# Kernel optimization log

Hardware: AMD Instinct MI355X
Metric: run time of the kernel (lower is better)

Reference implementation:

```python
import jax, jax.numpy as jnp
import numpy as np

HIDDEN = 16
N_CLASSES = 10
N_NODES = 100000
N_EDGES = 3200000
D_FEAT = 128
NEG_SLOPE = 0.1


def setup_inputs() -> dict:
    key = jax.random.key(0)
    k1, k2, k3 = jax.random.split(key, 3)
    features = jax.random.normal(k1, (N_NODES, D_FEAT), dtype=jnp.float32)
    edge_src = jax.random.randint(k2, (N_EDGES,), 0, N_NODES, dtype=jnp.int64)
    edge_dst = jax.random.randint(k3, (N_EDGES,), 0, N_NODES, dtype=jnp.int64)
    return {"features": features, "edge_src": edge_src, "edge_dst": edge_dst}


def reference(features, edge_src, edge_dst):
    # SpMM: h[v] = sum over edges (u->v) of features[u]   (binary adjacency)
    msgs = features[edge_src]                      # [E, F] irregular gather
    h = jax.ops.segment_sum(msgs, edge_dst, num_segments=N_NODES)  # [N, F]
    # x @ ones(F, HIDDEN): every column equals the row-sum of h
    r1 = jnp.sum(h, axis=-1)                       # [N]
    a1 = jax.nn.leaky_relu(r1, NEG_SLOPE)          # leaky relu, slope 0.1
    # x @ ones(HIDDEN, N_CLASSES): each class column = HIDDEN * a1
    r2 = HIDDEN * a1
    a2 = jax.nn.leaky_relu(r2, NEG_SLOPE)
    # x @ ones(N_CLASSES, 1) then .int() and flatten
    r3 = N_CLASSES * a2                            # [N]
    return r3.astype(jnp.int32).reshape(-1)
```

## Files before the change

kernel.cpp:

```cpp
#include <hip/hip_runtime.h>

#define N_NODES  100000
#define N_EDGES  3200000
#define D_FEAT   128
#define SLICE    33344
#define SLICE4   (SLICE / 4)
#define N_SLICES 3
#define MAX_B    85
#define EPT      8
#define TPB      1024
#define STRIDE   (TPB * EPT)

__device__ __forceinline__ unsigned short f2bf(float f) {
    union { float f; unsigned u; } c; c.f = f;
    unsigned r = c.u + 0x7FFFu + ((c.u >> 16) & 1u);
    return (unsigned short)(r >> 16);
}
__device__ __forceinline__ float bf2f(unsigned short h) {
    union { unsigned u; float f; } c; c.u = ((unsigned)h) << 16; return c.f;
}

__global__ void __launch_bounds__(256) rowsum_kernel(
    const float* __restrict__ feat,
    float* __restrict__ rowsum)
{
    const int gid = (int)(blockIdx.x * blockDim.x + threadIdx.x);
    const int row = gid >> 5;
    const int sub = gid & 31;
    if (row >= N_NODES) return;

    const float4 v = reinterpret_cast<const float4*>(
        feat + (size_t)row * D_FEAT)[sub];
    float s = (v.x + v.y) + (v.z + v.w);

    #pragma unroll
    for (int off = 16; off > 0; off >>= 1)
        s += __shfl_xor(s, off, 64);

    if (sub == 0) rowsum[row] = s;
}

__global__ void __launch_bounds__(TPB) scatter_kernel(
    const int* __restrict__ edge_src,
    const int* __restrict__ edge_dst,
    const float* __restrict__ rowsum,
    unsigned short* __restrict__ copies,
    int B, int epb)
{
    __shared__ float lds[SLICE];

    const int tid = (int)threadIdx.x;
    const int b   = (int)blockIdx.x;
    const int s   = (int)blockIdx.y;
    const int lo  = s * SLICE;
    const unsigned len = (unsigned)((N_NODES - lo < SLICE) ? (N_NODES - lo) : SLICE);

    float4 z; z.x = z.y = z.z = z.w = 0.0f;
    for (int i = tid; i < SLICE4; i += TPB)
        reinterpret_cast<float4*>(lds)[i] = z;
    __syncthreads();

    const int begin = b * epb;
    const int end   = (begin + epb < N_EDGES) ? begin + epb : N_EDGES;

    int eA = begin + tid * EPT;
    int eB = eA + STRIDE;

    int4 dA0, dA1, sA0, sA1, dB0, dB1, sB0, sB1;
    if (eA     < end) { dA0 = *(const int4*)(edge_dst + eA);     sA0 = *(const int4*)(edge_src + eA); }
    if (eA + 4 < end) { dA1 = *(const int4*)(edge_dst + eA + 4); sA1 = *(const int4*)(edge_src + eA + 4); }
    if (eB     < end) { dB0 = *(const int4*)(edge_dst + eB);     sB0 = *(const int4*)(edge_src + eB); }
    if (eB + 4 < end) { dB1 = *(const int4*)(edge_dst + eB + 4); sB1 = *(const int4*)(edge_src + eB + 4); }

    unsigned jA0, jA1, jA2, jA3, jA4, jA5, jA6, jA7;
    float    wA0, wA1, wA2, wA3, wA4, wA5, wA6, wA7;
    {
        const bool v0 = (eA < end), v1 = (eA + 4 < end);
        jA0 = v0 ? (unsigned)(dA0.x - lo) : 0xFFFFFFFFu;
        jA1 = v0 ? (unsigned)(dA0.y - lo) : 0xFFFFFFFFu;
        jA2 = v0 ? (unsigned)(dA0.z - lo) : 0xFFFFFFFFu;
        jA3 = v0 ? (unsigned)(dA0.w - lo) : 0xFFFFFFFFu;
        jA4 = v1 ? (unsigned)(dA1.x - lo) : 0xFFFFFFFFu;
        jA5 = v1 ? (unsigned)(dA1.y - lo) : 0xFFFFFFFFu;
        jA6 = v1 ? (unsigned)(dA1.z - lo) : 0xFFFFFFFFu;
        jA7 = v1 ? (unsigned)(dA1.w - lo) : 0xFFFFFFFFu;
        wA0 = (jA0 < len) ? rowsum[sA0.x] : 0.0f;
        wA1 = (jA1 < len) ? rowsum[sA0.y] : 0.0f;
        wA2 = (jA2 < len) ? rowsum[sA0.z] : 0.0f;
        wA3 = (jA3 < len) ? rowsum[sA0.w] : 0.0f;
        wA4 = (jA4 < len) ? rowsum[sA1.x] : 0.0f;
        wA5 = (jA5 < len) ? rowsum[sA1.y] : 0.0f;
        wA6 = (jA6 < len) ? rowsum[sA1.z] : 0.0f;
        wA7 = (jA7 < len) ? rowsum[sA1.w] : 0.0f;
    }

    while (eA < end) {
        const int eC = eB + STRIDE;
        int4 dC0, dC1, sC0, sC1;
        if (eC     < end) { dC0 = *(const int4*)(edge_dst + eC);     sC0 = *(const int4*)(edge_src + eC); }
        if (eC + 4 < end) { dC1 = *(const int4*)(edge_dst + eC + 4); sC1 = *(const int4*)(edge_src + eC + 4); }

        const bool v0 = (eB < end), v1 = (eB + 4 < end);
        unsigned jB0 = v0 ? (unsigned)(dB0.x - lo) : 0xFFFFFFFFu;
        unsigned jB1 = v0 ? (unsigned)(dB0.y - lo) : 0xFFFFFFFFu;
        unsigned jB2 = v0 ? (unsigned)(dB0.z - lo) : 0xFFFFFFFFu;
        unsigned jB3 = v0 ? (unsigned)(dB0.w - lo) : 0xFFFFFFFFu;
        unsigned jB4 = v1 ? (unsigned)(dB1.x - lo) : 0xFFFFFFFFu;
        unsigned jB5 = v1 ? (unsigned)(dB1.y - lo) : 0xFFFFFFFFu;
        unsigned jB6 = v1 ? (unsigned)(dB1.z - lo) : 0xFFFFFFFFu;
        unsigned jB7 = v1 ? (unsigned)(dB1.w - lo) : 0xFFFFFFFFu;
        float wB0 = (jB0 < len) ? rowsum[sB0.x] : 0.0f;
        float wB1 = (jB1 < len) ? rowsum[sB0.y] : 0.0f;
        float wB2 = (jB2 < len) ? rowsum[sB0.z] : 0.0f;
        float wB3 = (jB3 < len) ? rowsum[sB0.w] : 0.0f;
        float wB4 = (jB4 < len) ? rowsum[sB1.x] : 0.0f;
        float wB5 = (jB5 < len) ? rowsum[sB1.y] : 0.0f;
        float wB6 = (jB6 < len) ? rowsum[sB1.z] : 0.0f;
        float wB7 = (jB7 < len) ? rowsum[sB1.w] : 0.0f;

        if (jA0 < len) atomicAdd(&lds[jA0], wA0);
        if (jA1 < len) atomicAdd(&lds[jA1], wA1);
        if (jA2 < len) atomicAdd(&lds[jA2], wA2);
        if (jA3 < len) atomicAdd(&lds[jA3], wA3);
        if (jA4 < len) atomicAdd(&lds[jA4], wA4);
        if (jA5 < len) atomicAdd(&lds[jA5], wA5);
        if (jA6 < len) atomicAdd(&lds[jA6], wA6);
        if (jA7 < len) atomicAdd(&lds[jA7], wA7);

        eA = eB; eB = eC;
        dB0 = dC0; dB1 = dC1; sB0 = sC0; sB1 = sC1;
        jA0 = jB0; jA1 = jB1; jA2 = jB2; jA3 = jB3;
        jA4 = jB4; jA5 = jB5; jA6 = jB6; jA7 = jB7;
        wA0 = wB0; wA1 = wB1; wA2 = wB2; wA3 = wB3;
        wA4 = wB4; wA5 = wB5; wA6 = wB6; wA7 = wB7;
    }
    __syncthreads();

    unsigned short* __restrict__ dstp = copies + ((size_t)s * B + b) * SLICE;
    const int len4 = (int)len >> 2;
    for (int i = tid; i < len4; i += TPB) {
        const float4 v = reinterpret_cast<const float4*>(lds)[i];
        ushort4 o;
        o.x = f2bf(v.x); o.y = f2bf(v.y); o.z = f2bf(v.z); o.w = f2bf(v.w);
        reinterpret_cast<ushort4*>(dstp)[i] = o;
    }
}

__global__ void __launch_bounds__(256) reduce_final_kernel(
    const unsigned short* __restrict__ copies,
    int B,
    int* __restrict__ out)
{
    const int i4 = (int)(blockIdx.x * blockDim.x + threadIdx.x);
    if (i4 >= N_NODES / 4) return;

    const int s  = (i4 >= 2 * SLICE4) ? 2 : (i4 >= SLICE4 ? 1 : 0);
    const int j4 = i4 - s * SLICE4;

    float ax = 0.0f, ay = 0.0f, az = 0.0f, aw = 0.0f;
    const ushort4* base = reinterpret_cast<const ushort4*>(copies)
                        + (size_t)s * B * SLICE4 + j4;
    #pragma unroll 4
    for (int c = 0; c < B; ++c) {
        const ushort4 v = base[(size_t)c * SLICE4];
        ax += bf2f(v.x); ay += bf2f(v.y); az += bf2f(v.z); aw += bf2f(v.w);
    }

    auto act = [](float x) -> int {
        const float a1 = (x  > 0.0f) ? x  : 0.1f * x;
        const float r2 = 16.0f * a1;
        const float a2 = (r2 > 0.0f) ? r2 : 0.1f * r2;
        return (int)(10.0f * a2);
    };

    int4 o;
    o.x = act(ax); o.y = act(ay); o.z = act(az); o.w = act(aw);
    reinterpret_cast<int4*>(out)[i4] = o;
}

extern "C" void kernel_launch(void* const* d_in, const int* in_sizes, int n_in,
                              void* d_out, int out_size, void* d_ws, size_t ws_size,
                              hipStream_t stream)
{
    const float* feat     = (const float*)d_in[0];
    const int*   edge_src = (const int*)d_in[1];
    const int*   edge_dst = (const int*)d_in[2];
    int*         out      = (int*)d_out;

    float* rowsum = (float*)d_ws;
    unsigned short* copies = (unsigned short*)(rowsum + N_NODES);

    size_t avail = (ws_size > (size_t)N_NODES * 4) ? ws_size - (size_t)N_NODES * 4 : 0;
    int B = (int)(avail / ((size_t)N_SLICES * SLICE * 2));
    if (B > MAX_B) B = MAX_B;
    if (B < 1) B = 1;

    int epb = (N_EDGES + B - 1) / B;
    epb = (epb + 7) & ~7;

    {
        const int threads = 256;
        const long long total = (long long)N_NODES * 32;
        const int blocks = (int)((total + threads - 1) / threads);
        rowsum_kernel<<<blocks, threads, 0, stream>>>(feat, rowsum);
    }

    {
        dim3 grid(B, N_SLICES);
        scatter_kernel<<<grid, TPB, 0, stream>>>(edge_src, edge_dst, rowsum,
                                                 copies, B, epb);
    }

    {
        const int threads = 256;
        const int blocks = (N_NODES / 4 + threads - 1) / threads;
        reduce_final_kernel<<<blocks, threads, 0, stream>>>(copies, B, out);
    }
}
```

Measured before the change: 53.18 us.

## Fix chunk count at 80 and remap scatter blocks so XCDs share edge chunks

Replaces the workspace-derived chunk count with a fixed 80 chunks of 40000 edges, launched as a 1D grid of 240 blocks. Block IDs are remapped so the three slice blocks that read the same edge chunk land on the same XCD (round-robin dispatch of 8), meant to let them share that XCD's L2 for the edge and rowsum reads. Constant loop bounds in the reduce kernel also allow full compile-time trip counts. The change drops the ws_size check, so it assumes the workspace is large enough, and fewer chunks means more edges per block.

Result: faster. 50.93 us (-4.2%).

```diff
diff --git a/kernel.cpp b/kernel.cpp
--- a/kernel.cpp
+++ b/kernel.cpp
@@ -6,7 +6,8 @@
 #define SLICE    33344
 #define SLICE4   (SLICE / 4)
 #define N_SLICES 3
-#define MAX_B    85
+#define NCHUNK   80
+#define EPB      40000
 #define EPT      8
 #define TPB      1024
 #define STRIDE   (TPB * EPT)
@@ -44,15 +45,18 @@
     const int* __restrict__ edge_src,
     const int* __restrict__ edge_dst,
     const float* __restrict__ rowsum,
-    unsigned short* __restrict__ copies,
-    int B, int epb)
+    unsigned short* __restrict__ copies)
 {
     __shared__ float lds[SLICE];
 
-    const int tid = (int)threadIdx.x;
-    const int b   = (int)blockIdx.x;
-    const int s   = (int)blockIdx.y;
-    const int lo  = s * SLICE;
+    const int tid  = (int)threadIdx.x;
+    const int bid  = (int)blockIdx.x;
+    const int g    = bid / 24;
+    const int r    = bid % 24;
+    const int xcd  = r & 7;
+    const int s    = r >> 3;
+    const int b    = g * 8 + xcd;
+    const int lo   = s * SLICE;
     const unsigned len = (unsigned)((N_NODES - lo < SLICE) ? (N_NODES - lo) : SLICE);
 
     float4 z; z.x = z.y = z.z = z.w = 0.0f;
@@ -60,8 +64,8 @@
         reinterpret_cast<float4*>(lds)[i] = z;
     __syncthreads();
 
-    const int begin = b * epb;
-    const int end   = (begin + epb < N_EDGES) ? begin + epb : N_EDGES;
+    const int begin = b * EPB;
+    const int end   = (begin + EPB < N_EDGES) ? begin + EPB : N_EDGES;
 
     int eA = begin + tid * EPT;
     int eB = eA + STRIDE;
@@ -136,7 +140,7 @@
     }
     __syncthreads();
 
-    unsigned short* __restrict__ dstp = copies + ((size_t)s * B + b) * SLICE;
+    unsigned short* __restrict__ dstp = copies + ((size_t)s * NCHUNK + b) * SLICE;
     const int len4 = (int)len >> 2;
     for (int i = tid; i < len4; i += TPB) {
         const float4 v = reinterpret_cast<const float4*>(lds)[i];
@@ -148,7 +152,6 @@
 
 __global__ void __launch_bounds__(256) reduce_final_kernel(
     const unsigned short* __restrict__ copies,
-    int B,
     int* __restrict__ out)
 {
     const int i4 = (int)(blockIdx.x * blockDim.x + threadIdx.x);
@@ -159,9 +162,9 @@
 
     float ax = 0.0f, ay = 0.0f, az = 0.0f, aw = 0.0f;
     const ushort4* base = reinterpret_cast<const ushort4*>(copies)
-                        + (size_t)s * B * SLICE4 + j4;
+                        + (size_t)s * NCHUNK * SLICE4 + j4;
     #pragma unroll 4
-    for (int c = 0; c < B; ++c) {
+    for (int c = 0; c < NCHUNK; ++c) {
         const ushort4 v = base[(size_t)c * SLICE4];
         ax += bf2f(v.x); ay += bf2f(v.y); az += bf2f(v.z); aw += bf2f(v.w);
     }
@@ -190,14 +193,6 @@
     float* rowsum = (float*)d_ws;
     unsigned short* copies = (unsigned short*)(rowsum + N_NODES);
 
-    size_t avail = (ws_size > (size_t)N_NODES * 4) ? ws_size - (size_t)N_NODES * 4 : 0;
-    int B = (int)(avail / ((size_t)N_SLICES * SLICE * 2));
-    if (B > MAX_B) B = MAX_B;
-    if (B < 1) B = 1;
-
-    int epb = (N_EDGES + B - 1) / B;
-    epb = (epb + 7) & ~7;
-
     {
         const int threads = 256;
         const long long total = (long long)N_NODES * 32;
@@ -205,15 +200,12 @@
         rowsum_kernel<<<blocks, threads, 0, stream>>>(feat, rowsum);
     }
 
-    {
-        dim3 grid(B, N_SLICES);
-        scatter_kernel<<<grid, TPB, 0, stream>>>(edge_src, edge_dst, rowsum,
-                                                 copies, B, epb);
-    }
+    scatter_kernel<<<N_SLICES * NCHUNK, TPB, 0, stream>>>(edge_src, edge_dst,
+                                                          rowsum, copies);
 
     {
         const int threads = 256;
         const int blocks = (N_NODES / 4 + threads - 1) / threads;
-        reduce_final_kernel<<<blocks, threads, 0, stream>>>(copies, B, out);
-    }
-}
+        reduce_final_kernel<<<blocks, threads, 0, stream>>>(copies, out);
+    }
+}
```
